# Optimization experiments

Hardware: AMD Instinct MI355X
Metric: run time of the kernel (lower is better)

The kernel has to match this reference:

```python
import jax, jax.numpy as jnp
import numpy as np

V = 50257   # vocab size
E = 256     # embedding_dimension
D = 8       # key_query_reduced_dimensionality
H = 8       # no_of_attention_heads
L = 16      # no_of_blocks
B = 8       # batch
T = 512     # seq len == context_size
FF = 4 * E  # MLP hidden


def setup_inputs() -> dict:
    key = jax.random.key(0)
    ks = jax.random.split(key, 12)
    rn = lambda k, s: jax.random.normal(k, s, jnp.float32) * 0.02
    return {
        'tokens': jax.random.randint(ks[0], (B, T), 0, V),
        'ideal_value': jax.random.randint(ks[1], (B, T), 0, V),
        'tok_emb': rn(ks[2], (V, E)),
        'pos_emb': rn(ks[3], (T, E)),
        'Wq': rn(ks[4], (L, H, E, D)),
        'Wk': rn(ks[5], (L, H, E, D)),
        'Wv': rn(ks[6], (L, H, E, D)),
        'Wo': rn(ks[7], (L, H * D, E)),
        'bo': jnp.zeros((L, E), jnp.float32),
        'ln1_s': jnp.ones((L, E), jnp.float32),
        'ln1_b': jnp.zeros((L, E), jnp.float32),
        'W1': rn(ks[8], (L, E, FF)),
        'b1': jnp.zeros((L, FF), jnp.float32),
        'W2': rn(ks[9], (L, FF, E)),
        'b2': jnp.zeros((L, E), jnp.float32),
        'ln2_s': jnp.ones((L, E), jnp.float32),
        'ln2_b': jnp.zeros((L, E), jnp.float32),
        'lnf_s': jnp.ones((E,), jnp.float32),
        'lnf_b': jnp.zeros((E,), jnp.float32),
        'Wf': rn(ks[10], (E, V)),
        'bf': jnp.zeros((V,), jnp.float32),
    }


def _ln(x, s, b):
    m = x.mean(-1, keepdims=True)
    v = ((x - m) ** 2).mean(-1, keepdims=True)
    return (x - m) * jax.lax.rsqrt(v + 1e-5) * s + b


def reference(tokens, ideal_value, tok_emb, pos_emb, Wq, Wk, Wv, Wo, bo,
              ln1_s, ln1_b, W1, b1, W2, b2, ln2_s, ln2_b, lnf_s, lnf_b, Wf, bf):
    Bn, Tn = tokens.shape
    x = tok_emb[tokens] + pos_emb[:Tn]                      # [B,T,E]
    # faithful mask: masked_fill where transpose(tril(R))==0 -> keep upper triangle
    keep = jnp.triu(jnp.ones((D, D), bool))
    scale = jnp.float32(E) ** 0.5

    def block(x, p):
        wq, wk, wv, wo, bo_, s1, bb1, w1, bm1, w2, bm2, s2, bb2 = p
        h = _ln(x, s1, bb1)
        Q = jnp.einsum('bte,hed->bhtd', h, wq)              # [B,H,T,D]
        K = jnp.einsum('bte,hed->bhtd', h, wk)
        Vv = jnp.einsum('bte,hed->bhtd', h, wv)
        # R = K^T @ Q : feature-by-feature [B,H,D,D] (this repo's quirky attention)
        R = jnp.einsum('bhti,bhtj->bhij', K, Q) / scale
        R = jax.nn.softmax(jnp.where(keep, R, -jnp.inf), axis=-1)
        a = jnp.einsum('bhti,bhij->bhtj', Vv, R)            # V @ R, [B,H,T,D]
        a = a.transpose(0, 2, 1, 3).reshape(x.shape[0], x.shape[1], H * D)
        x = x + a @ wo + bo_                                # dropout is identity (eval)
        h2 = _ln(x, s2, bb2)
        x = x + jax.nn.relu(h2 @ w1 + bm1) @ w2 + bm2
        return x, None

    x, _ = jax.lax.scan(block, x, (Wq, Wk, Wv, Wo, bo, ln1_s, ln1_b,
                                   W1, b1, W2, b2, ln2_s, ln2_b))
    logits = (_ln(x, lnf_s, lnf_b) @ Wf + bf).reshape(-1, V)  # [B*T, V]
    tgt = ideal_value.reshape(-1)
    logp = jax.nn.log_softmax(logits, axis=-1)
    loss = -jnp.take_along_axis(logp, tgt[:, None], axis=1).mean()
    return logits, loss
```

## Files before the change

kernel.cpp:

```cpp
#include <hip/hip_runtime.h>
#include <math.h>

#define V_SZ 50257
#define NPAD 50304
#define NCB 393

typedef short s16x8 __attribute__((ext_vector_type(8)));
typedef ushort u16x4 __attribute__((ext_vector_type(4)));
typedef float f32x4 __attribute__((ext_vector_type(4)));

__device__ __forceinline__ ushort f2bf(float x) {
    union { float f; unsigned u; } v; v.f = x;
    unsigned r = v.u + 0x7FFF + ((v.u >> 16) & 1);
    return (ushort)(r >> 16);
}
__device__ __forceinline__ float bf2f(ushort u) {
    union { unsigned u; float f; } v; v.u = ((unsigned)u) << 16; return v.f;
}

__global__ __launch_bounds__(256) void gpt_embed_ln(const int* __restrict__ tokens,
                                                    const float* __restrict__ tok_emb,
                                                    const float* __restrict__ pos_emb,
                                                    const float* __restrict__ s, const float* __restrict__ b,
                                                    float* __restrict__ x, ushort* __restrict__ hb) {
    int wave = threadIdx.x >> 6, lane = threadIdx.x & 63;
    int row = blockIdx.x * 4 + wave;
    int t = row & 511;
    int tok = tokens[row];
    float4 te = ((const float4*)(tok_emb + tok * 256))[lane];
    float4 pe = ((const float4*)(pos_emb + t * 256))[lane];
    float4 v = make_float4(te.x + pe.x, te.y + pe.y, te.z + pe.z, te.w + pe.w);
    ((float4*)(x + row * 256))[lane] = v;
    float sum = v.x + v.y + v.z + v.w;
    #pragma unroll
    for (int off = 1; off < 64; off <<= 1) sum += __shfl_xor(sum, off);
    float mean = sum * (1.0f / 256.0f);
    float dx = v.x - mean, dy = v.y - mean, dz = v.z - mean, dw = v.w - mean;
    float vs = dx * dx + dy * dy + dz * dz + dw * dw;
    #pragma unroll
    for (int off = 1; off < 64; off <<= 1) vs += __shfl_xor(vs, off);
    float rstd = rsqrtf(vs * (1.0f / 256.0f) + 1e-5f);
    float4 sv = ((const float4*)s)[lane];
    float4 bv = ((const float4*)b)[lane];
    u16x4 o;
    o[0] = f2bf(dx * rstd * sv.x + bv.x);
    o[1] = f2bf(dy * rstd * sv.y + bv.y);
    o[2] = f2bf(dz * rstd * sv.z + bv.z);
    o[3] = f2bf(dw * rstd * sv.w + bv.w);
    *(u16x4*)&hb[row * 256 + lane * 4] = o;
}

__global__ __launch_bounds__(256) void cvt_transpose(const float* __restrict__ in, ushort* __restrict__ out,
                                                     int Kd, int Nd, int n_real,
                                                     int in_stride, int out_stride) {
    __shared__ __align__(16) ushort t[64][80];
    const float* inp = in + (size_t)blockIdx.z * in_stride;
    ushort* outp = out + (size_t)blockIdx.z * out_stride;
    int n0 = blockIdx.x * 64, k0 = blockIdx.y * 64;
    int tid = threadIdx.x;
    #pragma unroll
    for (int p = 0; p < 4; p++) {
        int lk = p * 16 + (tid >> 4);
        int ln = (tid & 15) * 4;
        int k = k0 + lk, n = n0 + ln;
        const float* rowp = inp + (size_t)k * Nd;
        float v0 = 0.f, v1 = 0.f, v2 = 0.f, v3 = 0.f;
        if (n + 0 < n_real) v0 = rowp[n + 0];
        if (n + 1 < n_real) v1 = rowp[n + 1];
        if (n + 2 < n_real) v2 = rowp[n + 2];
        if (n + 3 < n_real) v3 = rowp[n + 3];
        t[ln + 0][lk] = f2bf(v0);
        t[ln + 1][lk] = f2bf(v1);
        t[ln + 2][lk] = f2bf(v2);
        t[ln + 3][lk] = f2bf(v3);
    }
    __syncthreads();
    int ln = tid >> 2, kq = (tid & 3) * 16;
    ushort* op = outp + (size_t)(n0 + ln) * Kd + k0 + kq;
    *(s16x8*)&op[0] = *(const s16x8*)&t[ln][kq];
    *(s16x8*)&op[8] = *(const s16x8*)&t[ln][kq + 8];
}

__global__ __launch_bounds__(256) void cvt_qkv(const float* __restrict__ Wq, const float* __restrict__ Wk,
                                               const float* __restrict__ Wv, ushort* __restrict__ WqkvT) {
    int l = blockIdx.x, kind = blockIdx.y;
    const float* W = (kind == 0 ? Wq : (kind == 1 ? Wk : Wv)) + l * 16384;
    ushort* out = WqkvT + (size_t)l * 65536 + kind * 64 * 256;
    int tid = threadIdx.x;
    #pragma unroll 4
    for (int it = 0; it < 64; it++) {
        int idx = it * 256 + tid;
        int row = idx >> 8, e = idx & 255;
        int h = row >> 3, d = row & 7;
        out[row * 256 + e] = f2bf(W[h * 2048 + e * 8 + d]);
    }
    if (kind == 0) {
        ushort* zp = WqkvT + (size_t)l * 65536 + 192 * 256;
        #pragma unroll 4
        for (int it = 0; it < 64; it++) zp[it * 256 + tid] = 0;
    }
}

__global__ __launch_bounds__(512, 4) void gpt_pre(const ushort* __restrict__ hb,
                                                  const ushort* __restrict__ WqkvT,
                                                  ushort* __restrict__ Vb,
                                                  float* __restrict__ Rpart) {
    __shared__ __align__(16) ushort As[16 * 64];
    __shared__ __align__(16) ushort Bs[256 * 64];
    __shared__ float kqv[16][193];
    const int tid = threadIdx.x, lane = tid & 63, wn = tid >> 6;
    const int rows0 = blockIdx.x * 16;
    const int fr = lane & 15, fkb = (lane >> 4) * 16;
    const int arow = tid >> 3, ach = tid & 7;

    f32x4 acc[2];
    acc[0] = (f32x4)0.0f; acc[1] = (f32x4)0.0f;

    s16x8 ra, rb[4];
    if (tid < 128) ra = *(const s16x8*)&hb[(size_t)(rows0 + arow) * 256 + ach * 8];
    #pragma unroll
    for (int i = 0; i < 4; i++) {
        int u = tid + i * 512, r = u >> 3, ch = u & 7;
        rb[i] = *(const s16x8*)&WqkvT[(size_t)r * 256 + ch * 8];
    }
    #pragma unroll 1
    for (int kt = 0; kt < 4; kt++) {
        if (kt) __syncthreads();
        if (tid < 128)
            *(s16x8*)&As[arow * 64 + (((ach * 16) ^ ((arow & 7) << 4)) >> 1)] = ra;
        #pragma unroll
        for (int i = 0; i < 4; i++) {
            int u = tid + i * 512, r = u >> 3, ch = u & 7;
            *(s16x8*)&Bs[r * 64 + (((ch * 16) ^ ((r & 7) << 4)) >> 1)] = rb[i];
        }
        __syncthreads();
        if (kt < 3) {
            int k0 = (kt + 1) * 64;
            if (tid < 128) ra = *(const s16x8*)&hb[(size_t)(rows0 + arow) * 256 + k0 + ach * 8];
            #pragma unroll
            for (int i = 0; i < 4; i++) {
                int u = tid + i * 512, r = u >> 3, ch = u & 7;
                rb[i] = *(const s16x8*)&WqkvT[(size_t)r * 256 + k0 + ch * 8];
            }
        }
        #pragma unroll
        for (int kk = 0; kk < 2; kk++) {
            int kbyte = kk * 64 + fkb;
            s16x8 af = *(const s16x8*)&As[fr * 64 + ((kbyte ^ ((fr & 7) << 4)) >> 1)];
            #pragma unroll
            for (int n = 0; n < 2; n++) {
                int brow = wn * 32 + n * 16 + fr;
                s16x8 bfv = *(const s16x8*)&Bs[brow * 64 + ((kbyte ^ ((brow & 7) << 4)) >> 1)];
                acc[n] = __builtin_amdgcn_mfma_f32_16x16x32_bf16(af, bfv, acc[n], 0, 0, 0);
            }
        }
    }
    #pragma unroll
    for (int n = 0; n < 2; n++) {
        int col = wn * 32 + n * 16 + fr;
        if (col < 192) {
            #pragma unroll
            for (int r = 0; r < 4; r++)
                kqv[(lane >> 4) * 4 + r][col] = acc[n][r];
        }
    }
    __syncthreads();
    #pragma unroll
    for (int i = 0; i < 2; i++) {
        int u = tid + i * 512, t = u >> 6, hd = u & 63;
        Vb[(size_t)(rows0 + t) * 64 + hd] = f2bf(kqv[t][128 + hd]);
    }
    {
        int h = tid >> 6, i2 = (tid >> 3) & 7, j = tid & 7;
        float s = 0.0f;
        #pragma unroll
        for (int t = 0; t < 16; t++)
            s += kqv[t][64 + h * 8 + i2] * kqv[t][h * 8 + j];
        int bb = rows0 >> 9, part = (rows0 >> 4) & 31;
        Rpart[(size_t)(bb * 32 + part) * 512 + tid] = s;
    }
}

__global__ __launch_bounds__(512, 4) void gpt_post(
        const float* __restrict__ Rpart, const ushort* __restrict__ Vb,
        const ushort* __restrict__ WoT, const float* __restrict__ bo,
        const ushort* __restrict__ W1T, const float* __restrict__ b1,
        const ushort* __restrict__ W2T, const float* __restrict__ b2,
        const float* __restrict__ ls2, const float* __restrict__ lb2,
        const float* __restrict__ nls, const float* __restrict__ nlb,
        float* __restrict__ x, ushort* __restrict__ hbout) {
    __shared__ __align__(16) ushort Bs[256 * 64];
    __shared__ __align__(16) ushort ffs[16 * 1024];
    __shared__ __align__(16) ushort h2s[16 * 256];
    __shared__ __align__(16) ushort abl[16 * 64];
    __shared__ __align__(16) ushort Vl[16 * 64];
    __shared__ float Rs[512];
    __shared__ float red1[16][8], red2[16][8], mrow[16], rrow[16];

    const int tid = threadIdx.x, lane = tid & 63, wn = tid >> 6;
    const int rows0 = blockIdx.x * 16, b = rows0 >> 9;
    const int fr = lane & 15, fkb = (lane >> 4) * 16, rbase = (lane >> 4) * 4;
    int colv[2]; colv[0] = wn * 32 + fr; colv[1] = wn * 32 + 16 + fr;

    {
        const float* rp = Rpart + (size_t)b * 32 * 512 + tid;
        float s = 0.0f;
        #pragma unroll
        for (int p = 0; p < 32; p++) s += rp[p * 512];
        s *= (1.0f / 16.0f);
        int ii = (tid >> 3) & 7, j = tid & 7;
        float val = (j >= ii) ? s : -INFINITY;
        float m = val;
        #pragma unroll
        for (int off = 1; off < 8; off <<= 1) m = fmaxf(m, __shfl_xor(m, off, 8));
        float ex = __expf(val - m);
        float su = ex;
        #pragma unroll
        for (int off = 1; off < 8; off <<= 1) su += __shfl_xor(su, off, 8);
        Rs[tid] = ex / su;
    }
    #pragma unroll
    for (int i = 0; i < 2; i++) {
        int u = tid + i * 512, t = u >> 6, hd = u & 63;
        Vl[t * 64 + hd] = Vb[(size_t)(rows0 + t) * 64 + hd];
    }
    __syncthreads();
    #pragma unroll
    for (int i = 0; i < 2; i++) {
        int u = tid + i * 512, t = u >> 6, hd = u & 63, h = hd >> 3, j = hd & 7;
        float a = 0.0f;
        #pragma unroll
        for (int q = 0; q < 8; q++)
            a += bf2f(Vl[t * 64 + h * 8 + q]) * Rs[h * 64 + q * 8 + j];
        abl[t * 64 + (((hd * 2) ^ ((t & 7) << 4)) >> 1)] = f2bf(a);
    }
    s16x8 rbv[4];
    #pragma unroll
    for (int i = 0; i < 4; i++) {
        int u = tid + i * 512, r = u >> 3, ch = u & 7;
        rbv[i] = *(const s16x8*)&WoT[(size_t)r * 64 + ch * 8];
    }
    __syncthreads();
    #pragma unroll
    for (int i = 0; i < 4; i++) {
        int u = tid + i * 512, r = u >> 3, ch = u & 7;
        *(s16x8*)&Bs[r * 64 + (((ch * 16) ^ ((r & 7) << 4)) >> 1)] = rbv[i];
    }
    __syncthreads();
    f32x4 acc[2];
    acc[0] = (f32x4)0.0f; acc[1] = (f32x4)0.0f;
    #pragma unroll
    for (int kk = 0; kk < 2; kk++) {
        int kbyte = kk * 64 + fkb;
        s16x8 af = *(const s16x8*)&abl[fr * 64 + ((kbyte ^ ((fr & 7) << 4)) >> 1)];
        #pragma unroll
        for (int n = 0; n < 2; n++) {
            int brow = wn * 32 + n * 16 + fr;
            s16x8 bfv = *(const s16x8*)&Bs[brow * 64 + ((kbyte ^ ((brow & 7) << 4)) >> 1)];
            acc[n] = __builtin_amdgcn_mfma_f32_16x16x32_bf16(af, bfv, acc[n], 0, 0, 0);
        }
    }
    float xn[2][4];
    #pragma unroll
    for (int n = 0; n < 2; n++) {
        int col = colv[n];
        float bbv = bo[col];
        #pragma unroll
        for (int r = 0; r < 4; r++)
            xn[n][r] = acc[n][r] + bbv + x[(size_t)(rows0 + rbase + r) * 256 + col];
    }
    #pragma unroll
    for (int r = 0; r < 4; r++) {
        float s1 = xn[0][r] + xn[1][r];
        float s2 = xn[0][r] * xn[0][r] + xn[1][r] * xn[1][r];
        #pragma unroll
        for (int off = 1; off < 16; off <<= 1) {
            s1 += __shfl_xor(s1, off);
            s2 += __shfl_xor(s2, off);
        }
        if (fr == 0) { red1[rbase + r][wn] = s1; red2[rbase + r][wn] = s2; }
    }
    __syncthreads();
    if (tid < 16) {
        float s1 = 0.f, s2 = 0.f;
        #pragma unroll
        for (int w = 0; w < 8; w++) { s1 += red1[tid][w]; s2 += red2[tid][w]; }
        float mean = s1 * (1.0f / 256.0f);
        float var = s2 * (1.0f / 256.0f) - mean * mean;
        mrow[tid] = mean;
        rrow[tid] = rsqrtf(var + 1e-5f);
    }
    __syncthreads();
    #pragma unroll
    for (int n = 0; n < 2; n++) {
        int col = colv[n];
        float lsv = ls2[col], lbv = lb2[col];
        #pragma unroll
        for (int r = 0; r < 4; r++) {
            int rl = rbase + r;
            float hv = (xn[n][r] - mrow[rl]) * rrow[rl] * lsv + lbv;
            h2s[rl * 256 + (((col * 2) ^ ((rl & 7) << 4)) >> 1)] = f2bf(hv);
        }
    }
    #pragma unroll 1
    for (int c = 0; c < 4; c++) {
        const ushort* Bg = W1T + (size_t)c * 256 * 256;
        acc[0] = (f32x4)0.0f; acc[1] = (f32x4)0.0f;
        #pragma unroll
        for (int i = 0; i < 4; i++) {
            int u = tid + i * 512, r = u >> 3, ch = u & 7;
            rbv[i] = *(const s16x8*)&Bg[(size_t)r * 256 + ch * 8];
        }
        #pragma unroll 1
        for (int kt = 0; kt < 4; kt++) {
            __syncthreads();
            #pragma unroll
            for (int i = 0; i < 4; i++) {
                int u = tid + i * 512, r = u >> 3, ch = u & 7;
                *(s16x8*)&Bs[r * 64 + (((ch * 16) ^ ((r & 7) << 4)) >> 1)] = rbv[i];
            }
            __syncthreads();
            if (kt < 3) {
                int k0 = (kt + 1) * 64;
                #pragma unroll
                for (int i = 0; i < 4; i++) {
                    int u = tid + i * 512, r = u >> 3, ch = u & 7;
                    rbv[i] = *(const s16x8*)&Bg[(size_t)r * 256 + k0 + ch * 8];
                }
            }
            #pragma unroll
            for (int kk = 0; kk < 2; kk++) {
                int kbyte = kt * 128 + kk * 64 + fkb;
                s16x8 af = *(const s16x8*)&h2s[fr * 256 + ((kbyte ^ ((fr & 7) << 4)) >> 1)];
                int kb2 = kk * 64 + fkb;
                #pragma unroll
                for (int n = 0; n < 2; n++) {
                    int brow = wn * 32 + n * 16 + fr;
                    s16x8 bfv = *(const s16x8*)&Bs[brow * 64 + ((kb2 ^ ((brow & 7) << 4)) >> 1)];
                    acc[n] = __builtin_amdgcn_mfma_f32_16x16x32_bf16(af, bfv, acc[n], 0, 0, 0);
                }
            }
        }
        #pragma unroll
        for (int n = 0; n < 2; n++) {
            int col = c * 256 + colv[n];
            float bb1 = b1[col];
            #pragma unroll
            for (int r = 0; r < 4; r++) {
                int rl = rbase + r;
                ffs[rl * 1024 + (((col * 2) ^ ((rl & 7) << 4)) >> 1)] =
                    f2bf(fmaxf(acc[n][r] + bb1, 0.0f));
            }
        }
    }
    f32x4 a2[2];
    a2[0] = (f32x4)0.0f; a2[1] = (f32x4)0.0f;
    #pragma unroll
    for (int i = 0; i < 4; i++) {
        int u = tid + i * 512, r = u >> 3, ch = u & 7;
        rbv[i] = *(const s16x8*)&W2T[(size_t)r * 1024 + ch * 8];
    }
    #pragma unroll 1
    for (int kt = 0; kt < 16; kt++) {
        __syncthreads();
        #pragma unroll
        for (int i = 0; i < 4; i++) {
            int u = tid + i * 512, r = u >> 3, ch = u & 7;
            *(s16x8*)&Bs[r * 64 + (((ch * 16) ^ ((r & 7) << 4)) >> 1)] = rbv[i];
        }
        __syncthreads();
        if (kt < 15) {
            int k0 = (kt + 1) * 64;
            #pragma unroll
            for (int i = 0; i < 4; i++) {
                int u = tid + i * 512, r = u >> 3, ch = u & 7;
                rbv[i] = *(const s16x8*)&W2T[(size_t)r * 1024 + k0 + ch * 8];
            }
        }
        #pragma unroll
        for (int kk = 0; kk < 2; kk++) {
            int kbyte = kt * 128 + kk * 64 + fkb;
            s16x8 af = *(const s16x8*)&ffs[fr * 1024 + ((kbyte ^ ((fr & 7) << 4)) >> 1)];
            int kb2 = kk * 64 + fkb;
            #pragma unroll
            for (int n = 0; n < 2; n++) {
                int brow = wn * 32 + n * 16 + fr;
                s16x8 bfv = *(const s16x8*)&Bs[brow * 64 + ((kb2 ^ ((brow & 7) << 4)) >> 1)];
                a2[n] = __builtin_amdgcn_mfma_f32_16x16x32_bf16(af, bfv, a2[n], 0, 0, 0);
            }
        }
    }
    #pragma unroll
    for (int n = 0; n < 2; n++) {
        int col = colv[n];
        float bb2 = b2[col];
        #pragma unroll
        for (int r = 0; r < 4; r++) {
            float v = xn[n][r] + a2[n][r] + bb2;
            xn[n][r] = v;
            x[(size_t)(rows0 + rbase + r) * 256 + col] = v;
        }
    }
    __syncthreads();
    #pragma unroll
    for (int r = 0; r < 4; r++) {
        float s1 = xn[0][r] + xn[1][r];
        float s2 = xn[0][r] * xn[0][r] + xn[1][r] * xn[1][r];
        #pragma unroll
        for (int off = 1; off < 16; off <<= 1) {
            s1 += __shfl_xor(s1, off);
            s2 += __shfl_xor(s2, off);
        }
        if (fr == 0) { red1[rbase + r][wn] = s1; red2[rbase + r][wn] = s2; }
    }
    __syncthreads();
    if (tid < 16) {
        float s1 = 0.f, s2 = 0.f;
        #pragma unroll
        for (int w = 0; w < 8; w++) { s1 += red1[tid][w]; s2 += red2[tid][w]; }
        float mean = s1 * (1.0f / 256.0f);
        float var = s2 * (1.0f / 256.0f) - mean * mean;
        mrow[tid] = mean;
        rrow[tid] = rsqrtf(var + 1e-5f);
    }
    __syncthreads();
    #pragma unroll
    for (int n = 0; n < 2; n++) {
        int col = colv[n];
        float lsv = nls[col], lbv = nlb[col];
        #pragma unroll
        for (int r = 0; r < 4; r++) {
            int rl = rbase + r;
            hbout[(size_t)(rows0 + rl) * 256 + col] =
                f2bf((xn[n][r] - mrow[rl]) * rrow[rl] * lsv + lbv);
        }
    }
}

template<int K, int BM>
__device__ __forceinline__ void gemm_core(const ushort* __restrict__ A, const ushort* __restrict__ B,
                                          int row0, int c0, ushort* As, ushort* Bs, f32x4 acc[4][4]) {
    const int tid = threadIdx.x;
    const int lane = tid & 63;
    const int wid = tid >> 6;
    const int wm = wid >> 1, wn = wid & 1;
    const int srow = tid >> 3;
    const int schunk = tid & 7;
    constexpr int NA = BM / 32;
    constexpr int MR = BM / 32;

    #pragma unroll
    for (int m = 0; m < MR; m++)
        #pragma unroll
        for (int n = 0; n < 4; n++) acc[m][n] = (f32x4)0.0f;

    const int frow_a = wm * (BM / 2) + (lane & 15);
    const int frow_b = wn * 64 + (lane & 15);
    const int fk = (lane >> 4) * 16;
    const int sa = (frow_a & 7) << 4;
    const int sb = (frow_b & 7) << 4;

    s16x8 ra[NA], rb[4];
    #pragma unroll
    for (int i = 0; i < NA; i++)
        ra[i] = *(const s16x8*)&A[(size_t)(row0 + i * 32 + srow) * K + schunk * 8];
    #pragma unroll
    for (int i = 0; i < 4; i++)
        rb[i] = *(const s16x8*)&B[(size_t)(c0 + i * 32 + srow) * K + schunk * 8];

    const int nkt = K >> 6;
    #pragma unroll
    for (int kt = 0; kt < nkt; kt++) {
        if (kt) __syncthreads();
        #pragma unroll
        for (int i = 0; i < NA; i++) {
            int r = i * 32 + srow;
            int off = (schunk * 16) ^ ((r & 7) << 4);
            *(s16x8*)&As[r * 64 + (off >> 1)] = ra[i];
        }
        #pragma unroll
        for (int i = 0; i < 4; i++) {
            int r = i * 32 + srow;
            int off = (schunk * 16) ^ ((r & 7) << 4);
            *(s16x8*)&Bs[r * 64 + (off >> 1)] = rb[i];
        }
        __syncthreads();
        if (kt + 1 < nkt) {
            int k0 = (kt + 1) * 64;
            #pragma unroll
            for (int i = 0; i < NA; i++)
                ra[i] = *(const s16x8*)&A[(size_t)(row0 + i * 32 + srow) * K + k0 + schunk * 8];
            #pragma unroll
            for (int i = 0; i < 4; i++)
                rb[i] = *(const s16x8*)&B[(size_t)(c0 + i * 32 + srow) * K + k0 + schunk * 8];
        }
        #pragma unroll
        for (int kk = 0; kk < 2; kk++) {
            s16x8 af[MR], bfr[4];
            #pragma unroll
            for (int m = 0; m < MR; m++)
                af[m] = *(const s16x8*)&As[(frow_a + m * 16) * 64 + (((kk * 64 + fk) ^ sa) >> 1)];
            #pragma unroll
            for (int n = 0; n < 4; n++)
                bfr[n] = *(const s16x8*)&Bs[(frow_b + n * 16) * 64 + (((kk * 64 + fk) ^ sb) >> 1)];
            #pragma unroll
            for (int m = 0; m < MR; m++)
                #pragma unroll
                for (int n = 0; n < 4; n++)
                    acc[m][n] = __builtin_amdgcn_mfma_f32_16x16x32_bf16(af[m], bfr[n], acc[m][n], 0, 0, 0);
        }
    }
}

__global__ __launch_bounds__(256) void gpt_logits_mfma(const ushort* __restrict__ hb, const ushort* __restrict__ WfT,
                                                       const float* __restrict__ bfb, float* __restrict__ out,
                                                       float2* __restrict__ lsebuf) {
    __shared__ __align__(16) ushort As[128 * 64];
    __shared__ __align__(16) ushort Bs[128 * 64];
    f32x4 acc[4][4];
    int flat = blockIdx.y * 32 + blockIdx.x;
    int nf = (flat & 7) * 1572 + (flat >> 3);
    int rb = nf & 31, cb = nf >> 5;
    int row0 = rb * 128;
    int c0 = cb * 128;
    gemm_core<256, 128>(hb, WfT, row0, c0, As, Bs, acc);
    const int lane = threadIdx.x & 63, wid = threadIdx.x >> 6;
    const int wm = wid >> 1, wn = wid & 1;
    float bb[4]; int gcv[4];
    #pragma unroll
    for (int n = 0; n < 4; n++) {
        int gc = c0 + wn * 64 + n * 16 + (lane & 15);
        gcv[n] = gc;
        bb[n] = (gc < V_SZ) ? bfb[gc] : 0.0f;
    }
    __syncthreads();
    float2* red = (float2*)As;
    #pragma unroll
    for (int m = 0; m < 4; m++) {
        int gr = row0 + wm * 64 + m * 16 + (lane >> 4) * 4;
        #pragma unroll
        for (int r = 0; r < 4; r++) {
            float v[4];
            float vmax = -1e30f;
            #pragma unroll
            for (int n = 0; n < 4; n++) {
                v[n] = (gcv[n] < V_SZ) ? acc[m][n][r] + bb[n] : -1e30f;
                vmax = fmaxf(vmax, v[n]);
            }
            #pragma unroll
            for (int n = 0; n < 4; n++)
                if (gcv[n] < V_SZ)
                    out[(size_t)(gr + r) * V_SZ + gcv[n]] = v[n];
            #pragma unroll
            for (int off = 1; off < 16; off <<= 1)
                vmax = fmaxf(vmax, __shfl_xor(vmax, off));
            float vsum = __expf(v[0] - vmax) + __expf(v[1] - vmax)
                       + __expf(v[2] - vmax) + __expf(v[3] - vmax);
            #pragma unroll
            for (int off = 1; off < 16; off <<= 1)
                vsum += __shfl_xor(vsum, off);
            if ((lane & 15) == 0)
                red[(gr + r - row0) * 2 + wn] = make_float2(vmax, vsum);
        }
    }
    __syncthreads();
    if (threadIdx.x < 128) {
        float2 a = red[threadIdx.x * 2 + 0];
        float2 b = red[threadIdx.x * 2 + 1];
        float M = fmaxf(a.x, b.x);
        float S = a.y * __expf(a.x - M) + b.y * __expf(b.x - M);
        lsebuf[(size_t)(row0 + threadIdx.x) * NCB + cb] = make_float2(M, S);
    }
}

__global__ __launch_bounds__(256) void gpt_lse(const float2* __restrict__ lsebuf, const float* __restrict__ out,
                                               const int* __restrict__ tgt, float* __restrict__ partial) {
    int wave = threadIdx.x >> 6, lane = threadIdx.x & 63;
    int row = blockIdx.x * 4 + wave;
    float m = -INFINITY, s = 0.0f;
    for (int i = lane; i < NCB; i += 64) {
        float2 p = lsebuf[(size_t)row * NCB + i];
        float M = fmaxf(m, p.x);
        s = s * __expf(m - M) + p.y * __expf(p.x - M);
        m = M;
    }
    #pragma unroll
    for (int off = 1; off < 64; off <<= 1) {
        float m2 = __shfl_xor(m, off);
        float s2 = __shfl_xor(s, off);
        float M = fmaxf(m, m2);
        s = s * __expf(m - M) + s2 * __expf(m2 - M);
        m = M;
    }
    if (lane == 0)
        partial[row] = m + logf(s) - out[(size_t)row * V_SZ + tgt[row]];
}

__global__ void gpt_loss_reduce(const float* __restrict__ partial, float* __restrict__ out) {
    __shared__ float red[256];
    int tid = threadIdx.x;
    float s = 0.0f;
    for (int i = tid; i < 4096; i += 256) s += partial[i];
    red[tid] = s;
    __syncthreads();
    for (int off = 128; off > 0; off >>= 1) {
        if (tid < off) red[tid] += red[tid + off];
        __syncthreads();
    }
    if (tid == 0) out[0] = red[0] * (1.0f / 4096.0f);
}

__global__ void gpt_embed(const int* __restrict__ tokens, const float* __restrict__ tok_emb,
                          const float* __restrict__ pos_emb, float* __restrict__ x) {
    int idx = blockIdx.x * 256 + threadIdx.x;
    int bt = idx >> 8, e = idx & 255;
    int t = bt & 511;
    int tok = tokens[bt];
    x[idx] = tok_emb[tok * 256 + e] + pos_emb[t * 256 + e];
}

__global__ void gpt_ln(const float* __restrict__ x, const float* __restrict__ s,
                       const float* __restrict__ b, float* __restrict__ h) {
    __shared__ float red[256];
    int row = blockIdx.x, e = threadIdx.x;
    float v = x[row * 256 + e];
    red[e] = v;
    __syncthreads();
    for (int off = 128; off > 0; off >>= 1) {
        if (e < off) red[e] += red[e + off];
        __syncthreads();
    }
    float mean = red[0] * (1.0f / 256.0f);
    __syncthreads();
    float d = v - mean;
    red[e] = d * d;
    __syncthreads();
    for (int off = 128; off > 0; off >>= 1) {
        if (e < off) red[e] += red[e + off];
        __syncthreads();
    }
    float rstd = rsqrtf(red[0] * (1.0f / 256.0f) + 1e-5f);
    h[row * 256 + e] = d * rstd * s[e] + b[e];
}

__global__ void gpt_qkv(const float* __restrict__ h, const float* __restrict__ Wq,
                        const float* __restrict__ Wk, const float* __restrict__ Wv,
                        float* __restrict__ Q, float* __restrict__ K, float* __restrict__ Vv) {
    __shared__ float hs[8][256];
    int tid = threadIdx.x;
    int row0 = blockIdx.x * 8;
    #pragma unroll
    for (int r = 0; r < 8; r++) hs[r][tid] = h[(row0 + r) * 256 + tid];
    __syncthreads();
    if (tid < 192) {
        int kind = tid >> 6, o = tid & 63, hh = o >> 3, d = o & 7;
        const float* W = kind == 0 ? Wq : (kind == 1 ? Wk : Wv);
        const float* wp = W + hh * 2048 + d;
        float acc[8];
        #pragma unroll
        for (int r = 0; r < 8; r++) acc[r] = 0.0f;
        for (int e = 0; e < 256; e++) {
            float w = wp[e * 8];
            #pragma unroll
            for (int r = 0; r < 8; r++) acc[r] += hs[r][e] * w;
        }
        float* outp = kind == 0 ? Q : (kind == 1 ? K : Vv);
        int b = row0 >> 9;
        #pragma unroll
        for (int r = 0; r < 8; r++) {
            int t = (row0 + r) & 511;
            outp[((b * 8 + hh) * 512 + t) * 8 + d] = acc[r];
        }
    }
}

__global__ void gpt_attn_r(const float* __restrict__ K, const float* __restrict__ Q,
                           float* __restrict__ R) {
    __shared__ __align__(16) float Ks[64][8];
    __shared__ __align__(16) float Qs[64][8];
    int bh = blockIdx.x, tid = threadIdx.x;
    int i = tid >> 3, j = tid & 7;
    const float* Kb = K + bh * 512 * 8;
    const float* Qb = Q + bh * 512 * 8;
    float acc = 0.0f;
    for (int t0 = 0; t0 < 512; t0 += 64) {
        *(float4*)&Ks[tid][0] = *(const float4*)&Kb[(t0 + tid) * 8];
        *(float4*)&Ks[tid][4] = *(const float4*)&Kb[(t0 + tid) * 8 + 4];
        *(float4*)&Qs[tid][0] = *(const float4*)&Qb[(t0 + tid) * 8];
        *(float4*)&Qs[tid][4] = *(const float4*)&Qb[(t0 + tid) * 8 + 4];
        __syncthreads();
        #pragma unroll 16
        for (int t = 0; t < 64; t++) acc += Ks[t][i] * Qs[t][j];
        __syncthreads();
    }
    acc *= (1.0f / 16.0f);
    float val = (j >= i) ? acc : -INFINITY;
    float m = val;
    #pragma unroll
    for (int off = 1; off < 8; off <<= 1) m = fmaxf(m, __shfl_xor(m, off, 8));
    float ex = expf(val - m);
    float sum = ex;
    #pragma unroll
    for (int off = 1; off < 8; off <<= 1) sum += __shfl_xor(sum, off, 8);
    R[bh * 64 + tid] = ex / sum;
}

__global__ void gpt_attn_out(const float* __restrict__ Vv, const float* __restrict__ R,
                             const float* __restrict__ Wo, const float* __restrict__ bo,
                             float* __restrict__ x) {
    __shared__ __align__(16) float as[8][64];
    int tid = threadIdx.x;
    int row0 = blockIdx.x * 8;
    int b = row0 >> 9;
    #pragma unroll
    for (int k = 0; k < 2; k++) {
        int idx = k * 256 + tid;
        int r = idx >> 6, hd = idx & 63;
        int hh = hd >> 3, jj = hd & 7;
        int t = (row0 + r) & 511;
        const float* vp = Vv + ((b * 8 + hh) * 512 + t) * 8;
        const float* rp = R + (b * 8 + hh) * 64 + jj;
        float a = 0.0f;
        #pragma unroll
        for (int i = 0; i < 8; i++) a += vp[i] * rp[i * 8];
        as[r][hd] = a;
    }
    __syncthreads();
    float acc[8];
    float bb = bo[tid];
    #pragma unroll
    for (int r = 0; r < 8; r++) acc[r] = bb;
    for (int hd0 = 0; hd0 < 64; hd0 += 4) {
        float w0 = Wo[(hd0 + 0) * 256 + tid];
        float w1 = Wo[(hd0 + 1) * 256 + tid];
        float w2 = Wo[(hd0 + 2) * 256 + tid];
        float w3 = Wo[(hd0 + 3) * 256 + tid];
        #pragma unroll
        for (int r = 0; r < 8; r++) {
            float4 av = *(const float4*)&as[r][hd0];
            acc[r] += av.x * w0 + av.y * w1 + av.z * w2 + av.w * w3;
        }
    }
    #pragma unroll
    for (int r = 0; r < 8; r++) x[(row0 + r) * 256 + tid] += acc[r];
}

__global__ __launch_bounds__(256) void gpt_mlp(const float* __restrict__ h, const float* __restrict__ W1,
                         const float* __restrict__ b1, const float* __restrict__ W2,
                         const float* __restrict__ b2, float* __restrict__ x) {
    __shared__ __align__(16) float hs[8][256];
    __shared__ __align__(16) float ffs[8][1024];
    int tid = threadIdx.x;
    int row0 = blockIdx.x * 8;
    #pragma unroll
    for (int r = 0; r < 8; r++) hs[r][tid] = h[(row0 + r) * 256 + tid];
    __syncthreads();
    {
        float acc[4][8];
        #pragma unroll
        for (int k = 0; k < 4; k++) {
            float bb = b1[k * 256 + tid];
            #pragma unroll
            for (int r = 0; r < 8; r++) acc[k][r] = bb;
        }
        for (int e0 = 0; e0 < 256; e0 += 4) {
            float w[4][4];
            #pragma unroll
            for (int ee = 0; ee < 4; ee++)
                #pragma unroll
                for (int k = 0; k < 4; k++)
                    w[ee][k] = W1[(e0 + ee) * 1024 + k * 256 + tid];
            #pragma unroll
            for (int r = 0; r < 8; r++) {
                float4 hv = *(const float4*)&hs[r][e0];
                #pragma unroll
                for (int k = 0; k < 4; k++)
                    acc[k][r] += hv.x * w[0][k] + hv.y * w[1][k] + hv.z * w[2][k] + hv.w * w[3][k];
            }
        }
        #pragma unroll
        for (int k = 0; k < 4; k++)
            #pragma unroll
            for (int r = 0; r < 8; r++)
                ffs[r][k * 256 + tid] = fmaxf(acc[k][r], 0.0f);
    }
    __syncthreads();
    {
        float acc[8];
        float bb = b2[tid];
        #pragma unroll
        for (int r = 0; r < 8; r++) acc[r] = bb;
        for (int f0 = 0; f0 < 1024; f0 += 4) {
            float w0 = W2[(f0 + 0) * 256 + tid];
            float w1 = W2[(f0 + 1) * 256 + tid];
            float w2 = W2[(f0 + 2) * 256 + tid];
            float w3 = W2[(f0 + 3) * 256 + tid];
            #pragma unroll
            for (int r = 0; r < 8; r++) {
                float4 fv = *(const float4*)&ffs[r][f0];
                acc[r] += fv.x * w0 + fv.y * w1 + fv.z * w2 + fv.w * w3;
            }
        }
        #pragma unroll
        for (int r = 0; r < 8; r++) x[(row0 + r) * 256 + tid] += acc[r];
    }
}

__global__ __launch_bounds__(256) void gpt_logits(const float* __restrict__ hf, const float* __restrict__ Wf,
                            const float* __restrict__ bf, float* __restrict__ out) {
    __shared__ __align__(16) float hs[32][256];
    int tid = threadIdx.x;
    int row0 = blockIdx.y * 32;
    #pragma unroll
    for (int r = 0; r < 32; r++) hs[r][tid] = hf[(row0 + r) * 256 + tid];
    __syncthreads();
    int c0 = blockIdx.x * 512 + tid;
    int c1 = c0 + 256;
    int c0c = c0 < V_SZ ? c0 : V_SZ - 1;
    int c1c = c1 < V_SZ ? c1 : V_SZ - 1;
    float acc0[32], acc1[32];
    float b0 = bf[c0c], b1 = bf[c1c];
    #pragma unroll
    for (int r = 0; r < 32; r++) { acc0[r] = b0; acc1[r] = b1; }
    const float* p0 = Wf + c0c;
    const float* p1 = Wf + c1c;
    for (int e0 = 0; e0 < 256; e0 += 4) {
        float w00 = p0[(size_t)(e0 + 0) * V_SZ];
        float w01 = p0[(size_t)(e0 + 1) * V_SZ];
        float w02 = p0[(size_t)(e0 + 2) * V_SZ];
        float w03 = p0[(size_t)(e0 + 3) * V_SZ];
        float w10 = p1[(size_t)(e0 + 0) * V_SZ];
        float w11 = p1[(size_t)(e0 + 1) * V_SZ];
        float w12 = p1[(size_t)(e0 + 2) * V_SZ];
        float w13 = p1[(size_t)(e0 + 3) * V_SZ];
        #pragma unroll
        for (int r = 0; r < 32; r++) {
            float4 hv = *(const float4*)&hs[r][e0];
            acc0[r] += hv.x * w00 + hv.y * w01 + hv.z * w02 + hv.w * w03;
            acc1[r] += hv.x * w10 + hv.y * w11 + hv.z * w12 + hv.w * w13;
        }
    }
    if (c0 < V_SZ) {
        #pragma unroll
        for (int r = 0; r < 32; r++) out[(size_t)(row0 + r) * V_SZ + c0] = acc0[r];
    }
    if (c1 < V_SZ) {
        #pragma unroll
        for (int r = 0; r < 32; r++) out[(size_t)(row0 + r) * V_SZ + c1] = acc1[r];
    }
}

__global__ void gpt_loss(const float* __restrict__ logits, const int* __restrict__ tgt,
                         float* __restrict__ partial) {
    __shared__ float ms[256], ss[256];
    int row = blockIdx.x, tid = threadIdx.x;
    const float* lr = logits + (size_t)row * V_SZ;
    float m = -INFINITY, s = 0.0f;
    for (int c = tid; c < V_SZ; c += 256) {
        float v = lr[c];
        float nm = fmaxf(m, v);
        s = s * expf(m - nm) + expf(v - nm);
        m = nm;
    }
    ms[tid] = m; ss[tid] = s;
    __syncthreads();
    for (int off = 128; off > 0; off >>= 1) {
        if (tid < off) {
            float m2 = ms[tid + off], s2 = ss[tid + off];
            float M = fmaxf(ms[tid], m2);
            ss[tid] = ss[tid] * expf(ms[tid] - M) + s2 * expf(m2 - M);
            ms[tid] = M;
        }
        __syncthreads();
    }
    if (tid == 0) {
        float lse = ms[0] + logf(ss[0]);
        partial[row] = lse - lr[tgt[row]];
    }
}

extern "C" void kernel_launch(void* const* d_in, const int* in_sizes, int n_in,
                              void* d_out, int out_size, void* d_ws, size_t ws_size,
                              hipStream_t stream) {
    const int*   tokens  = (const int*)d_in[0];
    const int*   ideal   = (const int*)d_in[1];
    const float* tok_emb = (const float*)d_in[2];
    const float* pos_emb = (const float*)d_in[3];
    const float* Wq      = (const float*)d_in[4];
    const float* Wk      = (const float*)d_in[5];
    const float* Wv      = (const float*)d_in[6];
    const float* Wo      = (const float*)d_in[7];
    const float* bo      = (const float*)d_in[8];
    const float* ln1_s   = (const float*)d_in[9];
    const float* ln1_b   = (const float*)d_in[10];
    const float* W1      = (const float*)d_in[11];
    const float* b1      = (const float*)d_in[12];
    const float* W2      = (const float*)d_in[13];
    const float* b2      = (const float*)d_in[14];
    const float* ln2_s   = (const float*)d_in[15];
    const float* ln2_b   = (const float*)d_in[16];
    const float* lnf_s   = (const float*)d_in[17];
    const float* lnf_b   = (const float*)d_in[18];
    const float* Wf      = (const float*)d_in[19];
    const float* bf      = (const float*)d_in[20];
    float* out = (float*)d_out;

    size_t off = 0;
    char* wsc = (char*)d_ws;
    ushort* WfT   = (ushort*)(wsc + off); off += (size_t)NPAD * 256 * 2;
    ushort* W1T   = (ushort*)(wsc + off); off += (size_t)16 * 1024 * 256 * 2;
    ushort* W2T   = (ushort*)(wsc + off); off += (size_t)16 * 256 * 1024 * 2;
    ushort* WqkvT = (ushort*)(wsc + off); off += (size_t)16 * 256 * 256 * 2;
    ushort* WoT   = (ushort*)(wsc + off); off += (size_t)16 * 256 * 64 * 2;
    ushort* hb    = (ushort*)(wsc + off); off += (size_t)4096 * 256 * 2;
    ushort* Vb    = (ushort*)(wsc + off); off += (size_t)4096 * 64 * 2;
    float*  x     = (float*)(wsc + off);  off += (size_t)4096 * 256 * 4;
    float*  Rpart = (float*)(wsc + off);  off += (size_t)8 * 32 * 512 * 4;
    float*  partial = (float*)(wsc + off); off += (size_t)4096 * 4;
    float2* lsebuf = (float2*)(wsc + off); off += (size_t)4096 * NCB * 8;
    bool big = ws_size >= off;

    if (big) {
        cvt_transpose<<<dim3(16, 4, 16), 256, 0, stream>>>(W1, W1T, 256, 1024, 1024, 262144, 262144);
        cvt_transpose<<<dim3(4, 16, 16), 256, 0, stream>>>(W2, W2T, 1024, 256, 256, 262144, 262144);
        cvt_transpose<<<dim3(4, 1, 16), 256, 0, stream>>>(Wo, WoT, 64, 256, 256, 16384, 16384);
        cvt_transpose<<<dim3(786, 4, 1), 256, 0, stream>>>(Wf, WfT, 256, V_SZ, V_SZ, 0, 0);
        cvt_qkv<<<dim3(16, 3), 256, 0, stream>>>(Wq, Wk, Wv, WqkvT);

        gpt_embed_ln<<<1024, 256, 0, stream>>>(tokens, tok_emb, pos_emb, ln1_s, ln1_b, x, hb);

        for (int l = 0; l < 16; l++) {
            const float* nls = (l < 15) ? ln1_s + (l + 1) * 256 : lnf_s;
            const float* nlb = (l < 15) ? ln1_b + (l + 1) * 256 : lnf_b;
            gpt_pre<<<256, 512, 0, stream>>>(hb, WqkvT + (size_t)l * 65536, Vb, Rpart);
            gpt_post<<<256, 512, 0, stream>>>(Rpart, Vb,
                                              WoT + (size_t)l * 16384, bo + l * 256,
                                              W1T + (size_t)l * 262144, b1 + l * 1024,
                                              W2T + (size_t)l * 262144, b2 + l * 256,
                                              ln2_s + l * 256, ln2_b + l * 256,
                                              nls, nlb, x, hb);
        }

        gpt_logits_mfma<<<dim3(32, NCB), 256, 0, stream>>>(hb, WfT, bf, out, lsebuf);
        gpt_lse<<<1024, 256, 0, stream>>>(lsebuf, out, ideal, partial);
        gpt_loss_reduce<<<1, 256, 0, stream>>>(partial, out + (size_t)4096 * V_SZ);
    } else {
        float* fx  = (float*)d_ws;
        float* fh  = fx + 4096 * 256;
        float* fQ  = fh + 4096 * 256;
        float* fK  = fQ + 4096 * 64;
        float* fV  = fK + 4096 * 64;
        float* fR  = fV + 4096 * 64;
        float* fpart = fR + 64 * 64;
        gpt_embed<<<4096, 256, 0, stream>>>(tokens, tok_emb, pos_emb, fx);
        for (int l = 0; l < 16; l++) {
            gpt_ln<<<4096, 256, 0, stream>>>(fx, ln1_s + l * 256, ln1_b + l * 256, fh);
            gpt_qkv<<<512, 256, 0, stream>>>(fh, Wq + l * 16384, Wk + l * 16384, Wv + l * 16384, fQ, fK, fV);
            gpt_attn_r<<<64, 64, 0, stream>>>(fK, fQ, fR);
            gpt_attn_out<<<512, 256, 0, stream>>>(fV, fR, Wo + l * 16384, bo + l * 256, fx);
            gpt_ln<<<4096, 256, 0, stream>>>(fx, ln2_s + l * 256, ln2_b + l * 256, fh);
            gpt_mlp<<<512, 256, 0, stream>>>(fh, W1 + l * 262144, b1 + l * 1024, W2 + l * 262144, b2 + l * 256, fx);
        }
        gpt_ln<<<4096, 256, 0, stream>>>(fx, lnf_s, lnf_b, fh);
        dim3 lg(99, 128);
        gpt_logits<<<lg, 256, 0, stream>>>(fh, Wf, bf, out);
        gpt_loss<<<4096, 256, 0, stream>>>(out, ideal, fpart);
        gpt_loss_reduce<<<1, 256, 0, stream>>>(fpart, out + (size_t)4096 * V_SZ);
    }
}
```

Baseline: 1.049 ms.

## Fuse next layer's QKV projection into post-attention kernel; drop LDS staging in logits GEMM

Each layer's post kernel now also runs the next layer's QKV projection and K^T·Q partial reduction on its freshly normalized rows. Those rows stay in shared memory instead of going through hb, which removes one launch per layer and the hb round trip. Rpart and V buffers are ping-ponged so a layer does not overwrite the inputs it is still reading. Separately, the logits GEMM now loads MFMA fragments directly from global memory instead of staging through LDS tiles. That cuts LDS traffic and syncs, but risks poorer coalescing and more repeated global reads.

```diff
diff --git a/kernel.cpp b/kernel.cpp
--- a/kernel.cpp
+++ b/kernel.cpp
@@ -181,14 +181,17 @@
     }
 }
 
-__global__ __launch_bounds__(512, 4) void gpt_post(
-        const float* __restrict__ Rpart, const ushort* __restrict__ Vb,
+__global__ __launch_bounds__(512, 4) void gpt_layer(
+        const float* __restrict__ Rpart_in, const ushort* __restrict__ Vb_in,
         const ushort* __restrict__ WoT, const float* __restrict__ bo,
         const ushort* __restrict__ W1T, const float* __restrict__ b1,
         const ushort* __restrict__ W2T, const float* __restrict__ b2,
         const float* __restrict__ ls2, const float* __restrict__ lb2,
         const float* __restrict__ nls, const float* __restrict__ nlb,
-        float* __restrict__ x, ushort* __restrict__ hbout) {
+        float* __restrict__ x,
+        const ushort* __restrict__ WqkvT_next,
+        ushort* __restrict__ Vb_out, float* __restrict__ Rpart_out,
+        ushort* __restrict__ hbout, int mode) {
     __shared__ __align__(16) ushort Bs[256 * 64];
     __shared__ __align__(16) ushort ffs[16 * 1024];
     __shared__ __align__(16) ushort h2s[16 * 256];
@@ -203,7 +206,7 @@
     int colv[2]; colv[0] = wn * 32 + fr; colv[1] = wn * 32 + 16 + fr;
 
     {
-        const float* rp = Rpart + (size_t)b * 32 * 512 + tid;
+        const float* rp = Rpart_in + (size_t)b * 32 * 512 + tid;
         float s = 0.0f;
         #pragma unroll
         for (int p = 0; p < 32; p++) s += rp[p * 512];
@@ -222,7 +225,7 @@
     #pragma unroll
     for (int i = 0; i < 2; i++) {
         int u = tid + i * 512, t = u >> 6, hd = u & 63;
-        Vl[t * 64 + hd] = Vb[(size_t)(rows0 + t) * 64 + hd];
+        Vl[t * 64 + hd] = Vb_in[(size_t)(rows0 + t) * 64 + hd];
     }
     __syncthreads();
     #pragma unroll
@@ -431,110 +434,122 @@
         #pragma unroll
         for (int r = 0; r < 4; r++) {
             int rl = rbase + r;
-            hbout[(size_t)(rows0 + rl) * 256 + col] =
-                f2bf((xn[n][r] - mrow[rl]) * rrow[rl] * lsv + lbv);
-        }
-    }
-}
-
-template<int K, int BM>
-__device__ __forceinline__ void gemm_core(const ushort* __restrict__ A, const ushort* __restrict__ B,
-                                          int row0, int c0, ushort* As, ushort* Bs, f32x4 acc[4][4]) {
-    const int tid = threadIdx.x;
-    const int lane = tid & 63;
-    const int wid = tid >> 6;
-    const int wm = wid >> 1, wn = wid & 1;
-    const int srow = tid >> 3;
-    const int schunk = tid & 7;
-    constexpr int NA = BM / 32;
-    constexpr int MR = BM / 32;
-
-    #pragma unroll
-    for (int m = 0; m < MR; m++)
-        #pragma unroll
-        for (int n = 0; n < 4; n++) acc[m][n] = (f32x4)0.0f;
-
-    const int frow_a = wm * (BM / 2) + (lane & 15);
-    const int frow_b = wn * 64 + (lane & 15);
-    const int fk = (lane >> 4) * 16;
-    const int sa = (frow_a & 7) << 4;
-    const int sb = (frow_b & 7) << 4;
-
-    s16x8 ra[NA], rb[4];
-    #pragma unroll
-    for (int i = 0; i < NA; i++)
-        ra[i] = *(const s16x8*)&A[(size_t)(row0 + i * 32 + srow) * K + schunk * 8];
-    #pragma unroll
-    for (int i = 0; i < 4; i++)
-        rb[i] = *(const s16x8*)&B[(size_t)(c0 + i * 32 + srow) * K + schunk * 8];
-
-    const int nkt = K >> 6;
-    #pragma unroll
-    for (int kt = 0; kt < nkt; kt++) {
-        if (kt) __syncthreads();
-        #pragma unroll
-        for (int i = 0; i < NA; i++) {
-            int r = i * 32 + srow;
-            int off = (schunk * 16) ^ ((r & 7) << 4);
-            *(s16x8*)&As[r * 64 + (off >> 1)] = ra[i];
-        }
+            float hv = (xn[n][r] - mrow[rl]) * rrow[rl] * lsv + lbv;
+            ushort hu = f2bf(hv);
+            h2s[rl * 256 + (((col * 2) ^ ((rl & 7) << 4)) >> 1)] = hu;
+            if (mode == 0)
+                hbout[(size_t)(rows0 + rl) * 256 + col] = hu;
+        }
+    }
+    if (mode == 0) return;
+
+    float* kqv = (float*)ffs;
+    acc[0] = (f32x4)0.0f; acc[1] = (f32x4)0.0f;
+    #pragma unroll
+    for (int i = 0; i < 4; i++) {
+        int u = tid + i * 512, r = u >> 3, ch = u & 7;
+        rbv[i] = *(const s16x8*)&WqkvT_next[(size_t)r * 256 + ch * 8];
+    }
+    #pragma unroll 1
+    for (int kt = 0; kt < 4; kt++) {
+        __syncthreads();
         #pragma unroll
         for (int i = 0; i < 4; i++) {
-            int r = i * 32 + srow;
-            int off = (schunk * 16) ^ ((r & 7) << 4);
-            *(s16x8*)&Bs[r * 64 + (off >> 1)] = rb[i];
-        }
-        __syncthreads();
-        if (kt + 1 < nkt) {
+            int u = tid + i * 512, r = u >> 3, ch = u & 7;
+            *(s16x8*)&Bs[r * 64 + (((ch * 16) ^ ((r & 7) << 4)) >> 1)] = rbv[i];
+        }
+        __syncthreads();
+        if (kt < 3) {
             int k0 = (kt + 1) * 64;
             #pragma unroll
-            for (int i = 0; i < NA; i++)
-                ra[i] = *(const s16x8*)&A[(size_t)(row0 + i * 32 + srow) * K + k0 + schunk * 8];
-            #pragma unroll
-            for (int i = 0; i < 4; i++)
-                rb[i] = *(const s16x8*)&B[(size_t)(c0 + i * 32 + srow) * K + k0 + schunk * 8];
+            for (int i = 0; i < 4; i++) {
+                int u = tid + i * 512, r = u >> 3, ch = u & 7;
+                rbv[i] = *(const s16x8*)&WqkvT_next[(size_t)r * 256 + k0 + ch * 8];
+            }
         }
         #pragma unroll
         for (int kk = 0; kk < 2; kk++) {
-            s16x8 af[MR], bfr[4];
-            #pragma unroll
-            for (int m = 0; m < MR; m++)
-                af[m] = *(const s16x8*)&As[(frow_a + m * 16) * 64 + (((kk * 64 + fk) ^ sa) >> 1)];
-            #pragma unroll
-            for (int n = 0; n < 4; n++)
-                bfr[n] = *(const s16x8*)&Bs[(frow_b + n * 16) * 64 + (((kk * 64 + fk) ^ sb) >> 1)];
-            #pragma unroll
-            for (int m = 0; m < MR; m++)
-                #pragma unroll
-                for (int n = 0; n < 4; n++)
-                    acc[m][n] = __builtin_amdgcn_mfma_f32_16x16x32_bf16(af[m], bfr[n], acc[m][n], 0, 0, 0);
-        }
+            int kbyte = kt * 128 + kk * 64 + fkb;
+            s16x8 af = *(const s16x8*)&h2s[fr * 256 + ((kbyte ^ ((fr & 7) << 4)) >> 1)];
+            int kb2 = kk * 64 + fkb;
+            #pragma unroll
+            for (int n = 0; n < 2; n++) {
+                int brow = wn * 32 + n * 16 + fr;
+                s16x8 bfv = *(const s16x8*)&Bs[brow * 64 + ((kb2 ^ ((brow & 7) << 4)) >> 1)];
+                acc[n] = __builtin_amdgcn_mfma_f32_16x16x32_bf16(af, bfv, acc[n], 0, 0, 0);
+            }
+        }
+    }
+    __syncthreads();
+    #pragma unroll
+    for (int n = 0; n < 2; n++) {
+        int col = wn * 32 + n * 16 + fr;
+        if (col < 192) {
+            #pragma unroll
+            for (int r = 0; r < 4; r++)
+                kqv[(rbase + r) * 193 + col] = acc[n][r];
+        }
+    }
+    __syncthreads();
+    #pragma unroll
+    for (int i = 0; i < 2; i++) {
+        int u = tid + i * 512, t = u >> 6, hd = u & 63;
+        Vb_out[(size_t)(rows0 + t) * 64 + hd] = f2bf(kqv[t * 193 + 128 + hd]);
+    }
+    {
+        int h = tid >> 6, i2 = (tid >> 3) & 7, j = tid & 7;
+        float s = 0.0f;
+        #pragma unroll
+        for (int t = 0; t < 16; t++)
+            s += kqv[t * 193 + 64 + h * 8 + i2] * kqv[t * 193 + h * 8 + j];
+        int part = (rows0 >> 4) & 31;
+        Rpart_out[(size_t)(b * 32 + part) * 512 + tid] = s;
     }
 }
 
 __global__ __launch_bounds__(256) void gpt_logits_mfma(const ushort* __restrict__ hb, const ushort* __restrict__ WfT,
                                                        const float* __restrict__ bfb, float* __restrict__ out,
                                                        float2* __restrict__ lsebuf) {
-    __shared__ __align__(16) ushort As[128 * 64];
-    __shared__ __align__(16) ushort Bs[128 * 64];
+    __shared__ float2 redbuf[128][2];
     f32x4 acc[4][4];
     int flat = blockIdx.y * 32 + blockIdx.x;
     int nf = (flat & 7) * 1572 + (flat >> 3);
     int rb = nf & 31, cb = nf >> 5;
-    int row0 = rb * 128;
-    int c0 = cb * 128;
-    gemm_core<256, 128>(hb, WfT, row0, c0, As, Bs, acc);
+    int row0 = rb * 128, c0 = cb * 128;
     const int lane = threadIdx.x & 63, wid = threadIdx.x >> 6;
     const int wm = wid >> 1, wn = wid & 1;
+    const int fr = lane & 15;
+    const int kg = (lane >> 4) * 8;
+
+    #pragma unroll
+    for (int m = 0; m < 4; m++)
+        #pragma unroll
+        for (int n = 0; n < 4; n++) acc[m][n] = (f32x4)0.0f;
+
+    const ushort* Ab = hb  + (size_t)(row0 + wm * 64 + fr) * 256 + kg;
+    const ushort* Bb = WfT + (size_t)(c0  + wn * 64 + fr) * 256 + kg;
+    #pragma unroll
+    for (int ks = 0; ks < 8; ks++) {
+        s16x8 af[4], bfr[4];
+        #pragma unroll
+        for (int m = 0; m < 4; m++)
+            af[m] = *(const s16x8*)&Ab[(size_t)(m * 16) * 256 + ks * 32];
+        #pragma unroll
+        for (int n = 0; n < 4; n++)
+            bfr[n] = *(const s16x8*)&Bb[(size_t)(n * 16) * 256 + ks * 32];
+        #pragma unroll
+        for (int m = 0; m < 4; m++)
+            #pragma unroll
+            for (int n = 0; n < 4; n++)
+                acc[m][n] = __builtin_amdgcn_mfma_f32_16x16x32_bf16(af[m], bfr[n], acc[m][n], 0, 0, 0);
+    }
     float bb[4]; int gcv[4];
     #pragma unroll
     for (int n = 0; n < 4; n++) {
-        int gc = c0 + wn * 64 + n * 16 + (lane & 15);
+        int gc = c0 + wn * 64 + n * 16 + fr;
         gcv[n] = gc;
         bb[n] = (gc < V_SZ) ? bfb[gc] : 0.0f;
     }
-    __syncthreads();
-    float2* red = (float2*)As;
     #pragma unroll
     for (int m = 0; m < 4; m++) {
         int gr = row0 + wm * 64 + m * 16 + (lane >> 4) * 4;
@@ -560,13 +575,13 @@
             for (int off = 1; off < 16; off <<= 1)
                 vsum += __shfl_xor(vsum, off);
             if ((lane & 15) == 0)
-                red[(gr + r - row0) * 2 + wn] = make_float2(vmax, vsum);
+                redbuf[gr + r - row0][wn] = make_float2(vmax, vsum);
         }
     }
     __syncthreads();
     if (threadIdx.x < 128) {
-        float2 a = red[threadIdx.x * 2 + 0];
-        float2 b = red[threadIdx.x * 2 + 1];
+        float2 a = redbuf[threadIdx.x][0];
+        float2 b = redbuf[threadIdx.x][1];
         float M = fmaxf(a.x, b.x);
         float S = a.y * __expf(a.x - M) + b.y * __expf(b.x - M);
         lsebuf[(size_t)(row0 + threadIdx.x) * NCB + cb] = make_float2(M, S);
@@ -913,9 +928,11 @@
     ushort* WqkvT = (ushort*)(wsc + off); off += (size_t)16 * 256 * 256 * 2;
     ushort* WoT   = (ushort*)(wsc + off); off += (size_t)16 * 256 * 64 * 2;
     ushort* hb    = (ushort*)(wsc + off); off += (size_t)4096 * 256 * 2;
-    ushort* Vb    = (ushort*)(wsc + off); off += (size_t)4096 * 64 * 2;
+    ushort* Vb0   = (ushort*)(wsc + off); off += (size_t)4096 * 64 * 2;
+    ushort* Vb1   = (ushort*)(wsc + off); off += (size_t)4096 * 64 * 2;
     float*  x     = (float*)(wsc + off);  off += (size_t)4096 * 256 * 4;
-    float*  Rpart = (float*)(wsc + off);  off += (size_t)8 * 32 * 512 * 4;
+    float*  Rp0   = (float*)(wsc + off);  off += (size_t)8 * 32 * 512 * 4;
+    float*  Rp1   = (float*)(wsc + off);  off += (size_t)8 * 32 * 512 * 4;
     float*  partial = (float*)(wsc + off); off += (size_t)4096 * 4;
     float2* lsebuf = (float2*)(wsc + off); off += (size_t)4096 * NCB * 8;
     bool big = ws_size >= off;
@@ -928,17 +945,24 @@
         cvt_qkv<<<dim3(16, 3), 256, 0, stream>>>(Wq, Wk, Wv, WqkvT);
 
         gpt_embed_ln<<<1024, 256, 0, stream>>>(tokens, tok_emb, pos_emb, ln1_s, ln1_b, x, hb);
+        gpt_pre<<<256, 512, 0, stream>>>(hb, WqkvT, Vb0, Rp0);
 
         for (int l = 0; l < 16; l++) {
             const float* nls = (l < 15) ? ln1_s + (l + 1) * 256 : lnf_s;
             const float* nlb = (l < 15) ? ln1_b + (l + 1) * 256 : lnf_b;
-            gpt_pre<<<256, 512, 0, stream>>>(hb, WqkvT + (size_t)l * 65536, Vb, Rpart);
-            gpt_post<<<256, 512, 0, stream>>>(Rpart, Vb,
-                                              WoT + (size_t)l * 16384, bo + l * 256,
-                                              W1T + (size_t)l * 262144, b1 + l * 1024,
-                                              W2T + (size_t)l * 262144, b2 + l * 256,
-                                              ln2_s + l * 256, ln2_b + l * 256,
-                                              nls, nlb, x, hb);
+            const float* Rin = (l & 1) ? Rp1 : Rp0;
+            const ushort* Vin = (l & 1) ? Vb1 : Vb0;
+            float* Rout = (l & 1) ? Rp0 : Rp1;
+            ushort* Vout = (l & 1) ? Vb0 : Vb1;
+            int mode = (l < 15) ? 1 : 0;
+            const ushort* Wnext = WqkvT + (size_t)((l < 15) ? (l + 1) : 0) * 65536;
+            gpt_layer<<<256, 512, 0, stream>>>(Rin, Vin,
+                                               WoT + (size_t)l * 16384, bo + l * 256,
+                                               W1T + (size_t)l * 262144, b1 + l * 1024,
+                                               W2T + (size_t)l * 262144, b2 + l * 256,
+                                               ln2_s + l * 256, ln2_b + l * 256,
+                                               nls, nlb, x,
+                                               Wnext, Vout, Rout, hb, mode);
         }
 
         gpt_logits_mfma<<<dim3(32, NCB), 256, 0, stream>>>(hb, WfT, bf, out, lsebuf);
```

Result: slower. 1.138 ms (+8.5%).
